# Kernel tuning notes

Measured on AMD Instinct MI355X. Metric: run time of the kernel, lower is better.

Reference implementation:

```python
import jax, jax.numpy as jnp
import numpy as np
import math

D_MODEL = 2048
HEADS = 16
D_K = D_MODEL // HEADS  # 128
D_FF = 2048
N = 8192
EPS = 1e-6


def _norm(x, alpha, bias):
    # torch Norm: alpha * (x - mean) / (std + eps) + bias, std uses ddof=1
    mu = jnp.mean(x, axis=-1, keepdims=True)
    sd = jnp.std(x, axis=-1, ddof=1, keepdims=True)
    return alpha * (x - mu) / (sd + EPS) + bias


def setup_inputs() -> dict:
    key = jax.random.key(0)
    ks = jax.random.split(key, 16)
    s = 0.02
    inp = {
        "q": jax.random.normal(ks[0], (N, D_MODEL), jnp.float32),
        "k": jax.random.normal(ks[1], (N, D_MODEL), jnp.float32),
        "v": jax.random.normal(ks[2], (N, D_MODEL), jnp.float32),
        # norm params (norm_1 exists in module but is unused in forward)
        "nq_a": jnp.ones((D_MODEL,), jnp.float32), "nq_b": jnp.zeros((D_MODEL,), jnp.float32),
        "nk_a": jnp.ones((D_MODEL,), jnp.float32), "nk_b": jnp.zeros((D_MODEL,), jnp.float32),
        "nv_a": jnp.ones((D_MODEL,), jnp.float32), "nv_b": jnp.zeros((D_MODEL,), jnp.float32),
        "n2_a": jnp.ones((D_MODEL,), jnp.float32), "n2_b": jnp.zeros((D_MODEL,), jnp.float32),
        # attention projections, stored [in, out]
        "Wq": jax.random.normal(ks[3], (D_MODEL, D_MODEL), jnp.float32) * s,
        "bq": jnp.zeros((D_MODEL,), jnp.float32),
        "Wk": jax.random.normal(ks[4], (D_MODEL, D_MODEL), jnp.float32) * s,
        "bk": jnp.zeros((D_MODEL,), jnp.float32),
        "Wv": jax.random.normal(ks[5], (D_MODEL, D_MODEL), jnp.float32) * s,
        "bv": jnp.zeros((D_MODEL,), jnp.float32),
        "Wo": jax.random.normal(ks[6], (D_MODEL, D_MODEL), jnp.float32) * s,
        "bo": jnp.zeros((D_MODEL,), jnp.float32),
        # FFN
        "W1": jax.random.normal(ks[7], (D_MODEL, D_FF), jnp.float32) * s,
        "b1": jnp.zeros((D_FF,), jnp.float32),
        "W2": jax.random.normal(ks[8], (D_FF, D_MODEL), jnp.float32) * s,
        "b2": jnp.zeros((D_MODEL,), jnp.float32),
    }
    return inp


def reference(q, k, v,
              nq_a, nq_b, nk_a, nk_b, nv_a, nv_b, n2_a, n2_b,
              Wq, bq, Wk, bk, Wv, bv, Wo, bo, W1, b1, W2, b2):
    x = v  # residual stream (dropout is identity at inference)
    qn = _norm(q, nq_a, nq_b)
    kn = _norm(k, nk_a, nk_b)
    vn = _norm(v, nv_a, nv_b)

    # projections -> [N, h, d_k] then transpose(1,2) -> [N, d_k, h]
    qh = (qn @ Wq + bq).reshape(N, HEADS, D_K).transpose(0, 2, 1)
    kh = (kn @ Wk + bk).reshape(N, HEADS, D_K).transpose(0, 2, 1)
    vh = (vn @ Wv + bv).reshape(N, HEADS, D_K).transpose(0, 2, 1)

    # NON-STANDARD (as-written in source): per-token [d_k, d_k] attention
    # contracting over the head axis, scaled by 1/sqrt(d_k).
    scores = jnp.einsum('nah,nbh->nab', qh, kh) / math.sqrt(D_K)  # [N, d_k, d_k]
    probs = jax.nn.softmax(scores, axis=-1)
    attn = jnp.einsum('nab,nbh->nah', probs, vh)  # [N, d_k, h]

    concat = attn.transpose(0, 2, 1).reshape(N, D_MODEL)  # [N, h*d_k]
    x = x + (concat @ Wo + bo)

    x2 = _norm(x, n2_a, n2_b)
    ff = jax.nn.relu(x2 @ W1 + b1) @ W2 + b2
    return x + ff
```

## Files before the change

kernel.cpp:

```cpp
#include <hip/hip_runtime.h>
#include <hip/hip_bf16.h>

#define DM 2048
#define NTOK 8192
#define EPS 1e-6f

typedef __attribute__((ext_vector_type(8))) short short8;
typedef __attribute__((ext_vector_type(4))) short short4v;
typedef __attribute__((ext_vector_type(4))) float f32x4;
typedef __attribute__((ext_vector_type(16))) float f32x16;
typedef __attribute__((ext_vector_type(4))) unsigned int u32x4;

typedef const __attribute__((address_space(1))) void gvoid;
typedef __attribute__((address_space(3))) void lvoid;

static __device__ __forceinline__ unsigned short f2bf(float f) {
    unsigned u = __builtin_bit_cast(unsigned, f);
    unsigned r = u + 0x7FFFu + ((u >> 16) & 1u);
    return (unsigned short)(r >> 16);
}
static __device__ __forceinline__ float bf2f(unsigned short h) {
    return __builtin_bit_cast(float, (unsigned)h << 16);
}

__global__ __launch_bounds__(256) void norm_rows(
        const float* __restrict__ in, const float* __restrict__ alpha,
        const float* __restrict__ beta, unsigned short* __restrict__ out) {
    const int row = blockIdx.x;
    const int t = threadIdx.x;
    const float* x = in + (size_t)row * DM + t * 8;
    float4 v0 = *(const float4*)(x);
    float4 v1 = *(const float4*)(x + 4);
    float s = (v0.x + v0.y) + (v0.z + v0.w) + (v1.x + v1.y) + (v1.z + v1.w);
    float ss = v0.x*v0.x + v0.y*v0.y + v0.z*v0.z + v0.w*v0.w
             + v1.x*v1.x + v1.y*v1.y + v1.z*v1.z + v1.w*v1.w;
    #pragma unroll
    for (int m = 1; m < 64; m <<= 1) {
        s  += __shfl_xor(s, m);
        ss += __shfl_xor(ss, m);
    }
    __shared__ float red[8];
    const int wv = t >> 6, ln = t & 63;
    if (ln == 0) { red[wv] = s; red[4 + wv] = ss; }
    __syncthreads();
    s  = (red[0] + red[1]) + (red[2] + red[3]);
    ss = (red[4] + red[5]) + (red[6] + red[7]);
    const float mu = s * (1.0f / DM);
    float var = (ss - s * mu) * (1.0f / (DM - 1));
    var = fmaxf(var, 0.0f);
    const float scale = 1.0f / (sqrtf(var) + EPS);
    float4 a0 = *(const float4*)(alpha + t*8);
    float4 a1 = *(const float4*)(alpha + t*8 + 4);
    float4 b0 = *(const float4*)(beta + t*8);
    float4 b1 = *(const float4*)(beta + t*8 + 4);
    short8 o;
    o[0] = (short)f2bf(a0.x * (v0.x - mu) * scale + b0.x);
    o[1] = (short)f2bf(a0.y * (v0.y - mu) * scale + b0.y);
    o[2] = (short)f2bf(a0.z * (v0.z - mu) * scale + b0.z);
    o[3] = (short)f2bf(a0.w * (v0.w - mu) * scale + b0.w);
    o[4] = (short)f2bf(a1.x * (v1.x - mu) * scale + b1.x);
    o[5] = (short)f2bf(a1.y * (v1.y - mu) * scale + b1.y);
    o[6] = (short)f2bf(a1.z * (v1.z - mu) * scale + b1.z);
    o[7] = (short)f2bf(a1.w * (v1.w - mu) * scale + b1.w);
    *(short8*)(out + (size_t)row * DM + t * 8) = o;
}

__global__ __launch_bounds__(256) void norm_rows_bf16(
        const unsigned short* __restrict__ in, const float* __restrict__ alpha,
        const float* __restrict__ beta, unsigned short* __restrict__ out) {
    const int row = blockIdx.x;
    const int t = threadIdx.x;
    short8 rv = *(const short8*)(in + (size_t)row * DM + t * 8);
    float xv[8];
    #pragma unroll
    for (int j = 0; j < 8; ++j) xv[j] = bf2f((unsigned short)rv[j]);
    float s = 0.f, ss = 0.f;
    #pragma unroll
    for (int j = 0; j < 8; ++j) { s += xv[j]; ss += xv[j]*xv[j]; }
    #pragma unroll
    for (int m = 1; m < 64; m <<= 1) {
        s  += __shfl_xor(s, m);
        ss += __shfl_xor(ss, m);
    }
    __shared__ float red[8];
    const int wv = t >> 6, ln = t & 63;
    if (ln == 0) { red[wv] = s; red[4 + wv] = ss; }
    __syncthreads();
    s  = (red[0] + red[1]) + (red[2] + red[3]);
    ss = (red[4] + red[5]) + (red[6] + red[7]);
    const float mu = s * (1.0f / DM);
    float var = (ss - s * mu) * (1.0f / (DM - 1));
    var = fmaxf(var, 0.0f);
    const float scale = 1.0f / (sqrtf(var) + EPS);
    short8 o;
    #pragma unroll
    for (int j = 0; j < 8; ++j) {
        const float av = alpha[t*8 + j], bv = beta[t*8 + j];
        o[j] = (short)f2bf(av * (xv[j] - mu) * scale + bv);
    }
    *(short8*)(out + (size_t)row * DM + t * 8) = o;
}

__global__ __launch_bounds__(256) void wtrans6(
        const float* __restrict__ Wq, const float* __restrict__ Wk,
        const float* __restrict__ Wv, const float* __restrict__ Wo,
        const float* __restrict__ W1, const float* __restrict__ W2,
        unsigned short* __restrict__ Tq, unsigned short* __restrict__ Tk,
        unsigned short* __restrict__ Tv, unsigned short* __restrict__ To,
        unsigned short* __restrict__ T1, unsigned short* __restrict__ T2,
        float isq) {
    __shared__ float tile[32][33];
    const int z = blockIdx.z;
    const float* W = z==0?Wq: z==1?Wk: z==2?Wv: z==3?Wo: z==4?W1: W2;
    unsigned short* Wt = z==0?Tq: z==1?Tk: z==2?Tv: z==3?To: z==4?T1: T2;
    const int perm = (z < 2) ? 1 : 0;
    const float ws = (z == 0) ? isq : 1.0f;
    const int bc = blockIdx.x * 32, bk = blockIdx.y * 32;
    const int t = threadIdx.x;
    const int tc = t & 31, tr = t >> 5;
    #pragma unroll
    for (int i = 0; i < 4; ++i)
        tile[tr + i*8][tc] = W[(size_t)(bk + tr + i*8) * DM + bc + tc];
    __syncthreads();
    #pragma unroll
    for (int i = 0; i < 4; ++i) {
        const int c = bc + tr + i*8;
        const int pc = perm ? ((c & 127) * 16 + (c >> 7)) : c;
        Wt[(size_t)pc * DM + bk + tc] = f2bf(tile[tc][tr + i*8] * ws);
    }
}

#define BARRIER __builtin_amdgcn_s_barrier()
#define WAIT_LGKM0 asm volatile("s_waitcnt lgkmcnt(0)" ::: "memory")
#define VMCNT(n) asm volatile("s_waitcnt vmcnt(" #n ")" ::: "memory")
#define SCHED_FENCE __builtin_amdgcn_sched_barrier(0)

template<int EPI>
__global__ __launch_bounds__(512, 2) void gemm256(
        const unsigned short* __restrict__ A, const unsigned short* __restrict__ Bt,
        const float* __restrict__ bias, const float* __restrict__ residF,
        const unsigned short* __restrict__ residB,
        float* __restrict__ outF, unsigned short* __restrict__ outB, int biasPerm,
        float bscale) {
    __shared__ __align__(16) char lds[131072];
    char* ldsA = lds;
    char* ldsB = lds + 65536;

    const int t = threadIdx.x, l = t & 63, w = t >> 6;
    const int wm = w >> 2, wn = w & 3;

    const int b = blockIdx.x;
    const int xcd = b & 7;
    const int j = b >> 3;
    const int m0 = (xcd * 4 + (j & 3)) * 256;
    const int n0 = (j >> 2) * 256;

    const int rS = t >> 3;
    const int cS = ((t & 7) ^ (rS & 7)) * 8;
    const unsigned short* aSt = A  + (size_t)(m0 + rS) * 2048 + cS;
    const unsigned short* bSt = Bt + (size_t)(n0 + rS) * 2048 + cS;
    const int ldsStW = w * 1024;

    const int aRd = wm * 16384 + (l & 15) * 128;
    const int bRd = (wn >> 1) * 16384 + (wn & 1) * 8192 + (l & 15) * 128;
    const int ch0 = (((l >> 4) + 0) ^ (l & 7)) * 16;
    const int ch1 = (((l >> 4) + 4) ^ (l & 7)) * 16;

    short8 af[8][2], bf[4][2];
    f32x4 acc[8][4] = {};

#define STG_A(buf, h, kt) do { \
    __builtin_amdgcn_global_load_lds((gvoid*)(aSt + (size_t)((h)*128)*2048 + (kt)*64), \
        (lvoid*)(ldsA + (buf)*32768 + (h)*16384 + ldsStW), 16, 0, 0); \
    __builtin_amdgcn_global_load_lds((gvoid*)(aSt + (size_t)((h)*128+64)*2048 + (kt)*64), \
        (lvoid*)(ldsA + (buf)*32768 + (h)*16384 + 8192 + ldsStW), 16, 0, 0); \
} while(0)
#define STG_B(buf, h, kt) do { \
    __builtin_amdgcn_global_load_lds((gvoid*)(bSt + (size_t)((h)*128)*2048 + (kt)*64), \
        (lvoid*)(ldsB + (buf)*32768 + (h)*16384 + ldsStW), 16, 0, 0); \
    __builtin_amdgcn_global_load_lds((gvoid*)(bSt + (size_t)((h)*128+64)*2048 + (kt)*64), \
        (lvoid*)(ldsB + (buf)*32768 + (h)*16384 + 8192 + ldsStW), 16, 0, 0); \
} while(0)
#define RD_A(buf, mh) do { \
    _Pragma("unroll") for (int ml = 0; ml < 4; ++ml) { \
        af[(mh)*4+ml][0] = *(const short8*)(ldsA + (buf)*32768 + aRd + ((mh)*4+ml)*2048 + ch0); \
        af[(mh)*4+ml][1] = *(const short8*)(ldsA + (buf)*32768 + aRd + ((mh)*4+ml)*2048 + ch1); \
    } } while(0)
#define RD_B(buf, nh) do { \
    _Pragma("unroll") for (int nl = 0; nl < 2; ++nl) { \
        bf[(nh)*2+nl][0] = *(const short8*)(ldsB + (buf)*32768 + bRd + ((nh)*2+nl)*2048 + ch0); \
        bf[(nh)*2+nl][1] = *(const short8*)(ldsB + (buf)*32768 + bRd + ((nh)*2+nl)*2048 + ch1); \
    } } while(0)
#define MM_Q(mh, nh) do { \
    _Pragma("unroll") for (int ml = 0; ml < 4; ++ml) \
    _Pragma("unroll") for (int nl = 0; nl < 2; ++nl) { \
        acc[(mh)*4+ml][(nh)*2+nl] = __builtin_amdgcn_mfma_f32_16x16x32_bf16( \
            af[(mh)*4+ml][0], bf[(nh)*2+nl][0], acc[(mh)*4+ml][(nh)*2+nl], 0, 0, 0); \
        acc[(mh)*4+ml][(nh)*2+nl] = __builtin_amdgcn_mfma_f32_16x16x32_bf16( \
            af[(mh)*4+ml][1], bf[(nh)*2+nl][1], acc[(mh)*4+ml][(nh)*2+nl], 0, 0, 0); \
    } \
} while(0)

    STG_A(0, 0, 0); STG_A(0, 1, 0);
    STG_B(0, 0, 0); STG_B(0, 1, 0);
    STG_A(1, 0, 1); STG_A(1, 1, 1);
    VMCNT(4);
    BARRIER;

    #pragma unroll 1
    for (int i = 0; i < 16; ++i) {
        const int kt1 = 2*i + 1, k2 = 2*i + 2, k3 = 2*i + 3;
        const bool more = (i < 15);
        RD_A(0, 0); RD_A(0, 1); RD_B(0, 0);
        STG_B(1, 0, kt1); STG_B(1, 1, kt1);
        SCHED_FENCE;
        BARRIER; WAIT_LGKM0;
        __builtin_amdgcn_s_setprio(1);
        MM_Q(0, 0); MM_Q(1, 0);
        __builtin_amdgcn_s_setprio(0);
        BARRIER;
        RD_B(0, 1);
        if (more) { STG_A(0, 0, k2); STG_A(0, 1, k2); SCHED_FENCE; VMCNT(4); }
        else { SCHED_FENCE; VMCNT(0); }
        BARRIER; WAIT_LGKM0;
        __builtin_amdgcn_s_setprio(1);
        MM_Q(0, 1); MM_Q(1, 1);
        __builtin_amdgcn_s_setprio(0);
        BARRIER;
        RD_A(1, 0); RD_A(1, 1); RD_B(1, 0);
        if (more) { STG_B(0, 0, k2); STG_B(0, 1, k2); }
        SCHED_FENCE;
        BARRIER; WAIT_LGKM0;
        __builtin_amdgcn_s_setprio(1);
        MM_Q(0, 0); MM_Q(1, 0);
        __builtin_amdgcn_s_setprio(0);
        BARRIER;
        RD_B(1, 1);
        if (more) { STG_A(1, 0, k3); STG_A(1, 1, k3); SCHED_FENCE; VMCNT(4); }
        else { SCHED_FENCE; }
        BARRIER; WAIT_LGKM0;
        __builtin_amdgcn_s_setprio(1);
        MM_Q(0, 1); MM_Q(1, 1);
        __builtin_amdgcn_s_setprio(0);
        BARRIER;
    }

    unsigned short* cs = (unsigned short*)lds;
    #pragma unroll 1
    for (int pass = 0; pass < 2; ++pass) {
        BARRIER;
        if (wm == pass) {
            #pragma unroll
            for (int ni = 0; ni < 4; ++ni) {
                const int col = wn*64 + ni*16 + (l & 15);
                const int gcol = n0 + col;
                const int cb = biasPerm ? ((gcol >> 4) + (gcol & 15) * 128) : gcol;
                const float bvv = bias[cb] * bscale;
                #pragma unroll
                for (int mi = 0; mi < 8; ++mi) {
                    #pragma unroll
                    for (int r = 0; r < 4; ++r) {
                        const int row = mi*16 + (l >> 4)*4 + r;
                        float vv = acc[mi][ni][r] + bvv;
                        if (EPI == 1) vv = fmaxf(vv, 0.0f);
                        cs[row*260 + col] = f2bf(vv);
                    }
                }
            }
        }
        BARRIER;
        #pragma unroll
        for (int s = 0; s < 8; ++s) {
            const int row = (t >> 5) + s*16;
            const int seg = t & 31;
            short8 pk = *(const short8*)(cs + row*260 + seg*8);
            const int grow = m0 + pass*128 + row;
            const size_t gb = (size_t)grow * 2048 + n0 + seg*8;
            if (EPI == 3) {
                float4 r0 = *(const float4*)(residF + gb);
                float4 r1 = *(const float4*)(residF + gb + 4);
                short8 o;
                o[0] = (short)f2bf(bf2f((unsigned short)pk[0]) + r0.x);
                o[1] = (short)f2bf(bf2f((unsigned short)pk[1]) + r0.y);
                o[2] = (short)f2bf(bf2f((unsigned short)pk[2]) + r0.z);
                o[3] = (short)f2bf(bf2f((unsigned short)pk[3]) + r0.w);
                o[4] = (short)f2bf(bf2f((unsigned short)pk[4]) + r1.x);
                o[5] = (short)f2bf(bf2f((unsigned short)pk[5]) + r1.y);
                o[6] = (short)f2bf(bf2f((unsigned short)pk[6]) + r1.z);
                o[7] = (short)f2bf(bf2f((unsigned short)pk[7]) + r1.w);
                *(short8*)(outB + gb) = o;
            } else if (EPI == 4) {
                short8 rb = *(const short8*)(residB + gb);
                float4 o0, o1;
                o0.x = bf2f((unsigned short)pk[0]) + bf2f((unsigned short)rb[0]);
                o0.y = bf2f((unsigned short)pk[1]) + bf2f((unsigned short)rb[1]);
                o0.z = bf2f((unsigned short)pk[2]) + bf2f((unsigned short)rb[2]);
                o0.w = bf2f((unsigned short)pk[3]) + bf2f((unsigned short)rb[3]);
                o1.x = bf2f((unsigned short)pk[4]) + bf2f((unsigned short)rb[4]);
                o1.y = bf2f((unsigned short)pk[5]) + bf2f((unsigned short)rb[5]);
                o1.z = bf2f((unsigned short)pk[6]) + bf2f((unsigned short)rb[6]);
                o1.w = bf2f((unsigned short)pk[7]) + bf2f((unsigned short)rb[7]);
                *(float4*)(outF + gb) = o0;
                *(float4*)(outF + gb + 4) = o1;
            } else {
                *(short8*)(outB + gb) = pk;
            }
        }
    }
#undef STG_A
#undef STG_B
#undef RD_A
#undef RD_B
#undef MM_Q
}

__global__ __launch_bounds__(256) void attn_tok(
        const unsigned short* __restrict__ Qt, const unsigned short* __restrict__ Kt,
        const unsigned short* __restrict__ Vp, unsigned short* __restrict__ Cc) {
    const int n = blockIdx.x;
    const int t = threadIdx.x, w = t >> 6, l = t & 63;
    const int q31 = l & 31, hi = l >> 5;
    __shared__ __align__(16) unsigned short c_s[16 * 132];

    const size_t tb = (size_t)n * DM;
    const short8 qf = *(const short8*)(Qt + tb + (w*32 + q31)*16 + hi*8);
    short8 kf[4];
    #pragma unroll
    for (int bt = 0; bt < 4; ++bt)
        kf[bt] = *(const short8*)(Kt + tb + (bt*32 + q31)*16 + hi*8);
    short8 vf[8];
    #pragma unroll
    for (int ks = 0; ks < 8; ++ks)
        vf[ks] = *(const short8*)(Vp + tb + (q31 & 15)*128 + ks*16 + hi*8);

    const f32x16 z = {};
    f32x16 sc[4];
    #pragma unroll
    for (int bt = 0; bt < 4; ++bt)
        sc[bt] = __builtin_amdgcn_mfma_f32_32x32x16_bf16(kf[bt], qf, z, 0, 0, 0);

    float m0 = sc[0][0], m1 = sc[1][0], m2 = sc[2][0], m3 = sc[3][0];
    #pragma unroll
    for (int r = 1; r < 16; ++r) {
        m0 = fmaxf(m0, sc[0][r]); m1 = fmaxf(m1, sc[1][r]);
        m2 = fmaxf(m2, sc[2][r]); m3 = fmaxf(m3, sc[3][r]);
    }
    float mx = fmaxf(fmaxf(m0, m1), fmaxf(m2, m3));
    { float a2 = mx, b2 = mx;
      asm volatile("v_permlane32_swap_b32 %0, %1" : "+v"(a2), "+v"(b2));
      mx = fmaxf(a2, b2); }

    float p[4][16];
    float s0 = 0.f, s1 = 0.f, s2 = 0.f, s3 = 0.f;
    #pragma unroll
    for (int r = 0; r < 16; ++r) {
        p[0][r] = __expf(sc[0][r] - mx); s0 += p[0][r];
        p[1][r] = __expf(sc[1][r] - mx); s1 += p[1][r];
        p[2][r] = __expf(sc[2][r] - mx); s2 += p[2][r];
        p[3][r] = __expf(sc[3][r] - mx); s3 += p[3][r];
    }
    float sm = (s0 + s1) + (s2 + s3);
    { float a2 = sm, b2 = sm;
      asm volatile("v_permlane32_swap_b32 %0, %1" : "+v"(a2), "+v"(b2));
      sm = a2 + b2; }
    const float inv = __builtin_amdgcn_rcpf(sm);
    #pragma unroll
    for (int bt = 0; bt < 4; ++bt)
        #pragma unroll
        for (int r = 0; r < 16; ++r)
            p[bt][r] *= inv;

    f32x16 acc = {};
    #pragma unroll
    for (int ks = 0; ks < 8; ++ks) {
        const int bt = ks >> 1, r0 = (ks & 1) * 8;
        unsigned X0, Y0, X1, Y1;
        asm("v_cvt_pk_bf16_f32 %0, %1, %2" : "=v"(X0) : "v"(p[bt][r0+0]), "v"(p[bt][r0+1]));
        asm("v_cvt_pk_bf16_f32 %0, %1, %2" : "=v"(Y0) : "v"(p[bt][r0+4]), "v"(p[bt][r0+5]));
        asm("v_cvt_pk_bf16_f32 %0, %1, %2" : "=v"(X1) : "v"(p[bt][r0+2]), "v"(p[bt][r0+3]));
        asm("v_cvt_pk_bf16_f32 %0, %1, %2" : "=v"(Y1) : "v"(p[bt][r0+6]), "v"(p[bt][r0+7]));
        asm volatile("v_permlane32_swap_b32 %0, %1" : "+v"(X0), "+v"(Y0));
        asm volatile("v_permlane32_swap_b32 %0, %1" : "+v"(X1), "+v"(Y1));
        u32x4 pw; pw[0] = X0; pw[1] = X1; pw[2] = Y0; pw[3] = Y1;
        const short8 paf = __builtin_bit_cast(short8, pw);
        acc = __builtin_amdgcn_mfma_f32_32x32x16_bf16(paf, vf[ks], acc, 0, 0, 0);
    }

    if (q31 < 16) {
        #pragma unroll
        for (int rp = 0; rp < 8; ++rp) {
            const int r = rp * 2;
            const int a = (r & 3) + 8 * (r >> 2) + 4 * hi;
            unsigned pk;
            asm("v_cvt_pk_bf16_f32 %0, %1, %2" : "=v"(pk) : "v"(acc[r]), "v"(acc[r+1]));
            *(unsigned*)((char*)c_s + q31*264 + (w*32 + a)*2) = pk;
        }
    }
    __syncthreads();
    *(short8*)(Cc + tb + t*8) = *(const short8*)((char*)c_s + (t >> 4)*264 + (t & 15)*16);
}

extern "C" void kernel_launch(void* const* d_in, const int* in_sizes, int n_in,
                              void* d_out, int out_size, void* d_ws, size_t ws_size,
                              hipStream_t stream) {
    (void)in_sizes; (void)n_in; (void)out_size; (void)ws_size;
    const float* q    = (const float*)d_in[0];
    const float* k    = (const float*)d_in[1];
    const float* v    = (const float*)d_in[2];
    const float* nq_a = (const float*)d_in[3];
    const float* nq_b = (const float*)d_in[4];
    const float* nk_a = (const float*)d_in[5];
    const float* nk_b = (const float*)d_in[6];
    const float* nv_a = (const float*)d_in[7];
    const float* nv_b = (const float*)d_in[8];
    const float* n2_a = (const float*)d_in[9];
    const float* n2_b = (const float*)d_in[10];
    const float* Wq   = (const float*)d_in[11];
    const float* bq   = (const float*)d_in[12];
    const float* Wk   = (const float*)d_in[13];
    const float* bk   = (const float*)d_in[14];
    const float* Wv   = (const float*)d_in[15];
    const float* bv   = (const float*)d_in[16];
    const float* Wo   = (const float*)d_in[17];
    const float* bo   = (const float*)d_in[18];
    const float* W1   = (const float*)d_in[19];
    const float* b1   = (const float*)d_in[20];
    const float* W2   = (const float*)d_in[21];
    const float* b2   = (const float*)d_in[22];

    char* ws = (char*)d_ws;
    const size_t MB = 1024 * 1024;
    unsigned short* buf0 = (unsigned short*)(ws);
    unsigned short* QtB  = (unsigned short*)(ws + 32*MB);
    unsigned short* KtB  = (unsigned short*)(ws + 64*MB);
    unsigned short* VpB  = (unsigned short*)(ws + 96*MB);
    unsigned short* Wqt  = (unsigned short*)(ws + 128*MB);
    unsigned short* Wkt  = (unsigned short*)(ws + 136*MB);
    unsigned short* Wvt  = (unsigned short*)(ws + 144*MB);
    unsigned short* Wot  = (unsigned short*)(ws + 152*MB);
    unsigned short* W1t  = (unsigned short*)(ws + 160*MB);
    unsigned short* W2t  = (unsigned short*)(ws + 168*MB);
    unsigned short* x2   = QtB;
    unsigned short* h1   = KtB;
    unsigned short* xb   = VpB;
    float* x = (float*)d_out;

    const float isq = 0.088388347648318447f;

    dim3 b256(256);
    dim3 gT6(DM / 32, DM / 32, 6);
    wtrans6<<<gT6, b256, 0, stream>>>(Wq, Wk, Wv, Wo, W1, W2,
                                      Wqt, Wkt, Wvt, Wot, W1t, W2t, isq);

    dim3 gN(NTOK);
    dim3 gG(256);
    dim3 b512(512);

    norm_rows<<<gN, b256, 0, stream>>>(q, nq_a, nq_b, buf0);
    gemm256<0><<<gG, b512, 0, stream>>>(buf0, Wqt, bq, nullptr, nullptr, nullptr, QtB, 1, isq);
    norm_rows<<<gN, b256, 0, stream>>>(k, nk_a, nk_b, buf0);
    gemm256<0><<<gG, b512, 0, stream>>>(buf0, Wkt, bk, nullptr, nullptr, nullptr, KtB, 1, 1.0f);
    norm_rows<<<gN, b256, 0, stream>>>(v, nv_a, nv_b, buf0);
    gemm256<0><<<gG, b512, 0, stream>>>(buf0, Wvt, bv, nullptr, nullptr, nullptr, VpB, 0, 1.0f);
    attn_tok<<<gN, b256, 0, stream>>>(QtB, KtB, VpB, buf0);
    gemm256<3><<<gG, b512, 0, stream>>>(buf0, Wot, bo, v, nullptr, nullptr, xb, 0, 1.0f);
    norm_rows_bf16<<<gN, b256, 0, stream>>>(xb, n2_a, n2_b, x2);
    gemm256<1><<<gG, b512, 0, stream>>>(x2, W1t, b1, nullptr, nullptr, nullptr, h1, 0, 1.0f);
    gemm256<4><<<gG, b512, 0, stream>>>(h1, W2t, b2, nullptr, xb, x, nullptr, 0, 1.0f);
}
```

Baseline: 559.5 us.

## Batch Q/K/V norms and projection GEMMs into single launches

Merges the three per-input row-norm kernels into one launch over a z-dimension, and the three QKV projection GEMMs into one 768-block launch that selects operands by block index. Normalized K and V are staged in the output buffer as scratch so all three can coexist. This removes launch gaps and the tail inefficiency of three separate 256-block grids, letting the GPU fill all CUs with more concurrent work. It risks somewhat worse cache locality across the mixed operand sets and relies on the output buffer being safe to reuse as scratch before the final write.

Result: faster. 548.1 us (-2.0%).

```diff
diff --git a/kernel.cpp b/kernel.cpp
--- a/kernel.cpp
+++ b/kernel.cpp
@@ -23,9 +23,19 @@
     return __builtin_bit_cast(float, (unsigned)h << 16);
 }
 
-__global__ __launch_bounds__(256) void norm_rows(
-        const float* __restrict__ in, const float* __restrict__ alpha,
-        const float* __restrict__ beta, unsigned short* __restrict__ out) {
+__global__ __launch_bounds__(256) void norm3(
+        const float* __restrict__ q, const float* __restrict__ k, const float* __restrict__ v,
+        const float* __restrict__ qa, const float* __restrict__ qb,
+        const float* __restrict__ ka, const float* __restrict__ kb,
+        const float* __restrict__ va, const float* __restrict__ vb,
+        unsigned short* __restrict__ oq, unsigned short* __restrict__ ok,
+        unsigned short* __restrict__ ov) {
+    const int z = blockIdx.z;
+    const float* in    = z == 0 ? q  : z == 1 ? k  : v;
+    const float* alpha = z == 0 ? qa : z == 1 ? ka : va;
+    const float* beta  = z == 0 ? qb : z == 1 ? kb : vb;
+    unsigned short* out = z == 0 ? oq : z == 1 ? ok : ov;
+
     const int row = blockIdx.x;
     const int t = threadIdx.x;
     const float* x = in + (size_t)row * DM + t * 8;
@@ -136,12 +146,12 @@
 #define SCHED_FENCE __builtin_amdgcn_sched_barrier(0)
 
 template<int EPI>
-__global__ __launch_bounds__(512, 2) void gemm256(
+__device__ __forceinline__ void gemm_core(
         const unsigned short* __restrict__ A, const unsigned short* __restrict__ Bt,
         const float* __restrict__ bias, const float* __restrict__ residF,
         const unsigned short* __restrict__ residB,
         float* __restrict__ outF, unsigned short* __restrict__ outB, int biasPerm,
-        float bscale) {
+        float bscale, int blk) {
     __shared__ __align__(16) char lds[131072];
     char* ldsA = lds;
     char* ldsB = lds + 65536;
@@ -149,9 +159,8 @@
     const int t = threadIdx.x, l = t & 63, w = t >> 6;
     const int wm = w >> 2, wn = w & 3;
 
-    const int b = blockIdx.x;
-    const int xcd = b & 7;
-    const int j = b >> 3;
+    const int xcd = blk & 7;
+    const int j = blk >> 3;
     const int m0 = (xcd * 4 + (j & 3)) * 256;
     const int n0 = (j >> 2) * 256;
 
@@ -314,6 +323,36 @@
 #undef MM_Q
 }
 
+template<int EPI>
+__global__ __launch_bounds__(512, 2) void gemm256(
+        const unsigned short* __restrict__ A, const unsigned short* __restrict__ Bt,
+        const float* __restrict__ bias, const float* __restrict__ residF,
+        const unsigned short* __restrict__ residB,
+        float* __restrict__ outF, unsigned short* __restrict__ outB, int biasPerm,
+        float bscale) {
+    gemm_core<EPI>(A, Bt, bias, residF, residB, outF, outB, biasPerm, bscale, blockIdx.x);
+}
+
+__global__ __launch_bounds__(512, 2) void gemm_qkv(
+        const unsigned short* __restrict__ Aq, const unsigned short* __restrict__ Ak,
+        const unsigned short* __restrict__ Av,
+        const unsigned short* __restrict__ Bq, const unsigned short* __restrict__ Bk,
+        const unsigned short* __restrict__ Bv,
+        const float* __restrict__ bq, const float* __restrict__ bk,
+        const float* __restrict__ bv,
+        unsigned short* __restrict__ Oq, unsigned short* __restrict__ Ok,
+        unsigned short* __restrict__ Ov, float isq) {
+    const int z = blockIdx.x >> 8;
+    const int blk = blockIdx.x & 255;
+    const unsigned short* A  = z == 0 ? Aq : z == 1 ? Ak : Av;
+    const unsigned short* Bt = z == 0 ? Bq : z == 1 ? Bk : Bv;
+    const float* bias        = z == 0 ? bq : z == 1 ? bk : bv;
+    unsigned short* outB     = z == 0 ? Oq : z == 1 ? Ok : Ov;
+    const int biasPerm = (z < 2) ? 1 : 0;
+    const float bscale = (z == 0) ? isq : 1.0f;
+    gemm_core<0>(A, Bt, bias, nullptr, nullptr, nullptr, outB, biasPerm, bscale, blk);
+}
+
 __global__ __launch_bounds__(256) void attn_tok(
         const unsigned short* __restrict__ Qt, const unsigned short* __restrict__ Kt,
         const unsigned short* __restrict__ Vp, unsigned short* __restrict__ Cc) {
@@ -444,6 +483,8 @@
     unsigned short* h1   = KtB;
     unsigned short* xb   = VpB;
     float* x = (float*)d_out;
+    unsigned short* knB = (unsigned short*)d_out;
+    unsigned short* vnB = knB + 16u*1024u*1024u;
 
     const float isq = 0.088388347648318447f;
 
@@ -452,16 +493,17 @@
     wtrans6<<<gT6, b256, 0, stream>>>(Wq, Wk, Wv, Wo, W1, W2,
                                       Wqt, Wkt, Wvt, Wot, W1t, W2t, isq);
 
+    dim3 gN3(NTOK, 1, 3);
+    norm3<<<gN3, b256, 0, stream>>>(q, k, v, nq_a, nq_b, nk_a, nk_b, nv_a, nv_b,
+                                    buf0, knB, vnB);
+
+    dim3 gQKV(768);
+    dim3 b512(512);
+    gemm_qkv<<<gQKV, b512, 0, stream>>>(buf0, knB, vnB, Wqt, Wkt, Wvt,
+                                        bq, bk, bv, QtB, KtB, VpB, isq);
+
     dim3 gN(NTOK);
     dim3 gG(256);
-    dim3 b512(512);
-
-    norm_rows<<<gN, b256, 0, stream>>>(q, nq_a, nq_b, buf0);
-    gemm256<0><<<gG, b512, 0, stream>>>(buf0, Wqt, bq, nullptr, nullptr, nullptr, QtB, 1, isq);
-    norm_rows<<<gN, b256, 0, stream>>>(k, nk_a, nk_b, buf0);
-    gemm256<0><<<gG, b512, 0, stream>>>(buf0, Wkt, bk, nullptr, nullptr, nullptr, KtB, 1, 1.0f);
-    norm_rows<<<gN, b256, 0, stream>>>(v, nv_a, nv_b, buf0);
-    gemm256<0><<<gG, b512, 0, stream>>>(buf0, Wvt, bv, nullptr, nullptr, nullptr, VpB, 0, 1.0f);
     attn_tok<<<gN, b256, 0, stream>>>(QtB, KtB, VpB, buf0);
     gemm256<3><<<gG, b512, 0, stream>>>(buf0, Wot, bo, v, nullptr, nullptr, xb, 0, 1.0f);
     norm_rows_bf16<<<gN, b256, 0, stream>>>(xb, n2_a, n2_b, x2);
```
